# Optimization experiments

Measured on AMD Instinct MI355X. Metric: run time of the kernel, lower is better.

The kernel has to match this reference:

```python
import jax, jax.numpy as jnp
import numpy as np
from jax import lax

B, T, D = 4096, 2048, 8
NUM_LAYERS = 6  # hidden_size = 1


def setup_inputs() -> dict:
    key = jax.random.key(0)
    ks = jax.random.split(key, 6)
    u = lambda k, shape: jax.random.uniform(k, shape, jnp.float32, -1.0, 1.0)  # pytorch init: U(-1/sqrt(H), 1/sqrt(H)), H=1
    return {
        "x": jax.random.normal(ks[0], (B, T, D), jnp.float32),
        "W_ih0": u(ks[1], (3, D)),            # layer 0 input weights [3*H, D], H=1
        "W_ih_rest": u(ks[2], (NUM_LAYERS - 1, 3)),  # layers 1..5 input weights [3*H, 1] squeezed
        "W_hh": u(ks[3], (NUM_LAYERS, 3)),    # hidden weights [3*H, H] squeezed (H=1)
        "b_ih": u(ks[4], (NUM_LAYERS, 3)),
        "b_hh": u(ks[5], (NUM_LAYERS, 3)),
    }


def _gru_layer(xp, w_hh, b_hh):
    # xp: [B, T, 3] precomputed input-gate projections (W_ih @ x + b_ih)
    # w_hh, b_hh: [3] scalar hidden weights/biases (hidden_size == 1)
    def step(h, xp_t):  # h: [B], xp_t: [B, 3]
        r = jax.nn.sigmoid(xp_t[:, 0] + w_hh[0] * h + b_hh[0])
        z = jax.nn.sigmoid(xp_t[:, 1] + w_hh[1] * h + b_hh[1])
        n = jnp.tanh(xp_t[:, 2] + r * (w_hh[2] * h + b_hh[2]))
        h_new = (1.0 - z) * n + z * h
        return h_new, h_new

    h0 = jnp.zeros(xp.shape[0], xp.dtype)
    _, ys = lax.scan(step, h0, jnp.swapaxes(xp, 0, 1))  # ys: [T, B]
    return jnp.swapaxes(ys, 0, 1)  # [B, T]


def reference(x, W_ih0, W_ih_rest, W_hh, b_ih, b_hh):
    # Layer 0: project D-dim input to the 3 gates once, then scan over time.
    xp = jnp.einsum('btd,gd->btg', x, W_ih0) + b_ih[0]  # [B, T, 3]
    h_seq = _gru_layer(xp, W_hh[0], b_hh[0])            # [B, T]
    # Layers 1..5: scalar input (previous layer's hidden), hidden_size=1.
    # Dropout(0.5) between layers is inference-mode identity here.
    for l in range(1, NUM_LAYERS):
        xp = h_seq[:, :, None] * W_ih_rest[l - 1][None, None, :] + b_ih[l]  # [B, T, 3]
        h_seq = _gru_layer(xp, W_hh[l], b_hh[l])
    # y[:, -1, 0] -> last timestep of last layer
    return h_seq[:, -1]
```

## Files before the change

### kernel.cpp

```cpp
#include <hip/hip_runtime.h>


#define T_LEN 2048
#define T8    (T_LEN * 8)
#define NCH   256

typedef __attribute__((ext_vector_type(2))) float v2f;

__device__ __forceinline__ float dpp_shr1(float v) {
    int i = __builtin_bit_cast(int, v);
    int r = __builtin_amdgcn_update_dpp(0, i, 0x111, 0xF, 0xF, true);
    return __builtin_bit_cast(float, r);
}

#define DPPSHL(S, v) __builtin_bit_cast(float,                                \
    __builtin_amdgcn_update_dpp(0, __builtin_bit_cast(int, (v)),              \
                                0x100 | ((S) == 0 ? 1 : (S)), 0xF, 0xF, true))
#define DPPSHLX(S, v) ((S) == 0 ? (v) : DPPSHL(S, v))

__global__ __launch_bounds__(64)
__attribute__((amdgpu_waves_per_eu(1, 1)))
void gru_scan(const float* __restrict__ x,
              const float* __restrict__ Wih0,
              const float* __restrict__ Wrest,
              const float* __restrict__ Whh,
              const float* __restrict__ bih,
              const float* __restrict__ bhh,
              float* __restrict__ out)
{
    const int lane = threadIdx.x & 63;
    const int l    = lane & 7;
    const int g    = lane >> 3;
    const int b    = blockIdx.x * 8 + g;

    const float c1 = -1.44269504088896340736f;
    const float cz =  1.44269504088896340736f;
    const float c2 = 2.0f * c1;

    const int  lidx = l < 6 ? l : 5;
    const bool lz   = (l == 0);
    const float m1  = lz ? 0.0f : 1.0f;

    const float whpr = c1 * Whh[lidx * 3 + 0];
    const float whpz = cz * Whh[lidx * 3 + 1];
    const float whpn = c2 * Whh[lidx * 3 + 2];
    const float bhpn = c2 * bhh[lidx * 3 + 2];
    const v2f  WH12 = {whpr, whpz};

    const int ir = lidx >= 1 ? lidx - 1 : 0;
    const float W1r = m1 * c1 * Wrest[ir * 3 + 0];
    const float W1z = m1 * cz * Wrest[ir * 3 + 1];
    const float W1n = m1 * c2 * Wrest[ir * 3 + 2];
    const v2f  W1rz = {W1r, W1z};
    const float B1r = c1 * (bih[lidx * 3 + 0] + bhh[lidx * 3 + 0]);
    const float B1z = cz * (bih[lidx * 3 + 1] + bhh[lidx * 3 + 1]);
    const float B1n = c2 *  bih[lidx * 3 + 2];
    const v2f  B1rz = {B1r, B1z};

    const v2f  B0rz = {c1 * (bih[0] + bhh[0]), cz * (bih[1] + bhh[1])};
    const float B0n = c2 * bih[2];
    v2f  wrz[8];
    float wn[8];
    #pragma unroll
    for (int d = 0; d < 8; ++d) {
        wrz[d] = (v2f){c1 * Wih0[d], cz * Wih0[8 + d]};
        wn[d]  = c2 * Wih0[16 + d];
    }

    const float4* xp = reinterpret_cast<const float4*>(x + (size_t)b * T8) + (lane & 7) * 2;

    float4 L0a, L0b, L1a, L1b, L2a, L2b, L3a, L3b;
    v2f   PZArz, PZBrz;
    float PZAn,  PZBn;
    v2f   SrzA[8], SrzB[8];
    float SnA[8],  SnB[8];
    float h = 0.0f;

#define LOADL(A, B, C)                                                        \
    { const int cc_ = ((C) < NCH) ? (C) : 0;                                  \
      const float4* p_ = xp + (size_t)cc_ * 16;                               \
      A = p_[0]; B = p_[1]; }

#define GETF(S, A, B) ((S)==0?(A).x:(S)==1?(A).y:(S)==2?(A).z:(S)==3?(A).w:  \
                       (S)==4?(B).x:(S)==5?(B).y:(S)==6?(B).z:(B).w)

#define DOT_SLICE(S, LA, LB, PRZ, PN)                                         \
    { const float xv_ = GETF(S, LA, LB);                                      \
      if ((S) == 0) { PRZ = wrz[0] * (v2f){xv_, xv_} + B0rz;                  \
                      PN  = fmaf(xv_, wn[0], B0n); }                          \
      else          { PRZ = wrz[S] * (v2f){xv_, xv_} + PRZ;                   \
                      PN  = fmaf(xv_, wn[S], PN); } }

#define PRESEL(S, SRZ, SN, PRZs, PNs)                                         \
    { const float br_ = DPPSHLX(S, (PRZs).x);                                 \
      const float bz_ = DPPSHLX(S, (PRZs).y);                                 \
      const float bn_ = DPPSHLX(S, (PNs));                                    \
      SRZ[S] = (v2f){lz ? br_ : B1r, lz ? bz_ : B1z};                         \
      SN[S]  = lz ? bn_ : B1n; }

    auto step1 = [&](int i, v2f brz, float bn, bool guard) {
        const float nbr = dpp_shr1(h);

        const v2f t12 = WH12 * (v2f){h, h} + brz;
        const v2f arz = W1rz * (v2f){nbr, nbr} + t12;
        const float er = __builtin_amdgcn_exp2f(arz.x);
        const float ez = __builtin_amdgcn_exp2f(arz.y);
        const float r  = __builtin_amdgcn_rcpf(1.0f + er);
        const float pz1 = 1.0f + ez;

        const v2f tnx = (v2f){whpn, W1n} * (v2f){h, nbr} + (v2f){bhpn, bn};
        const float na = fmaf(r, tnx.x, tnx.y);
        const float en = __builtin_amdgcn_exp2f(na);

        const float P  = fmaf(en, pz1, pz1);
        const float R  = __builtin_amdgcn_rcpf(P);
        const float hp1 = h + 1.0f;
        const float hm1 = 1.0f - h;
        const float q  = fmaf(-hp1, en, hm1);
        const float hn = fmaf(R, q, h);

        if (guard) {
            h = ((unsigned)(i - l) < (unsigned)T_LEN) ? hn : h;
        } else {
            h = hn;
        }
    };

#define STEPX(S, C, SRr, SNr, SRw, SNw, PZr_rz, PZr_n, PZw_rz, PZw_n,         \
              LNa, LNb, GD)                                                   \
    { step1((C) * 8 + (S), SRr[S], SNr[S], GD);                               \
      DOT_SLICE(S, LNa, LNb, PZw_rz, PZw_n)                                   \
      PRESEL(S, SRw, SNw, PZr_rz, PZr_n) }

#define RUN_CHUNK(C, SRr, SNr, SRw, SNw, PZr_rz, PZr_n, PZw_rz, PZw_n,        \
                  LNa, LNb, LlA, LlB, C4, GD)                                 \
    { LOADL(LlA, LlB, C4)                                                     \
      STEPX(0, C, SRr, SNr, SRw, SNw, PZr_rz, PZr_n, PZw_rz, PZw_n, LNa, LNb, GD) \
      STEPX(1, C, SRr, SNr, SRw, SNw, PZr_rz, PZr_n, PZw_rz, PZw_n, LNa, LNb, GD) \
      STEPX(2, C, SRr, SNr, SRw, SNw, PZr_rz, PZr_n, PZw_rz, PZw_n, LNa, LNb, GD) \
      STEPX(3, C, SRr, SNr, SRw, SNw, PZr_rz, PZr_n, PZw_rz, PZw_n, LNa, LNb, GD) \
      STEPX(4, C, SRr, SNr, SRw, SNw, PZr_rz, PZr_n, PZw_rz, PZw_n, LNa, LNb, GD) \
      STEPX(5, C, SRr, SNr, SRw, SNw, PZr_rz, PZr_n, PZw_rz, PZw_n, LNa, LNb, GD) \
      STEPX(6, C, SRr, SNr, SRw, SNw, PZr_rz, PZr_n, PZw_rz, PZw_n, LNa, LNb, GD) \
      STEPX(7, C, SRr, SNr, SRw, SNw, PZr_rz, PZr_n, PZw_rz, PZw_n, LNa, LNb, GD) }

    LOADL(L0a, L0b, 0) LOADL(L1a, L1b, 1) LOADL(L2a, L2b, 2) LOADL(L3a, L3b, 3)

    DOT_SLICE(0, L0a, L0b, PZArz, PZAn) DOT_SLICE(1, L0a, L0b, PZArz, PZAn)
    DOT_SLICE(2, L0a, L0b, PZArz, PZAn) DOT_SLICE(3, L0a, L0b, PZArz, PZAn)
    DOT_SLICE(4, L0a, L0b, PZArz, PZAn) DOT_SLICE(5, L0a, L0b, PZArz, PZAn)
    DOT_SLICE(6, L0a, L0b, PZArz, PZAn) DOT_SLICE(7, L0a, L0b, PZArz, PZAn)

    DOT_SLICE(0, L1a, L1b, PZBrz, PZBn) DOT_SLICE(1, L1a, L1b, PZBrz, PZBn)
    DOT_SLICE(2, L1a, L1b, PZBrz, PZBn) DOT_SLICE(3, L1a, L1b, PZBrz, PZBn)
    DOT_SLICE(4, L1a, L1b, PZBrz, PZBn) DOT_SLICE(5, L1a, L1b, PZBrz, PZBn)
    DOT_SLICE(6, L1a, L1b, PZBrz, PZBn) DOT_SLICE(7, L1a, L1b, PZBrz, PZBn)

    PRESEL(0, SrzA, SnA, PZArz, PZAn) PRESEL(1, SrzA, SnA, PZArz, PZAn)
    PRESEL(2, SrzA, SnA, PZArz, PZAn) PRESEL(3, SrzA, SnA, PZArz, PZAn)
    PRESEL(4, SrzA, SnA, PZArz, PZAn) PRESEL(5, SrzA, SnA, PZArz, PZAn)
    PRESEL(6, SrzA, SnA, PZArz, PZAn) PRESEL(7, SrzA, SnA, PZArz, PZAn)

    RUN_CHUNK(0, SrzA, SnA, SrzB, SnB, PZBrz, PZBn, PZArz, PZAn, L2a, L2b, L0a, L0b, 4, true)
    RUN_CHUNK(1, SrzB, SnB, SrzA, SnA, PZArz, PZAn, PZBrz, PZBn, L3a, L3b, L1a, L1b, 5, false)
    RUN_CHUNK(2, SrzA, SnA, SrzB, SnB, PZBrz, PZBn, PZArz, PZAn, L0a, L0b, L2a, L2b, 6, false)
    RUN_CHUNK(3, SrzB, SnB, SrzA, SnA, PZArz, PZAn, PZBrz, PZBn, L1a, L1b, L3a, L3b, 7, false)

    #pragma unroll 1
    for (int q = 1; q < 64; ++q) {
        const int c0 = q * 4;
        RUN_CHUNK(c0 + 0, SrzA, SnA, SrzB, SnB, PZBrz, PZBn, PZArz, PZAn, L2a, L2b, L0a, L0b, c0 + 4, false)
        RUN_CHUNK(c0 + 1, SrzB, SnB, SrzA, SnA, PZArz, PZAn, PZBrz, PZBn, L3a, L3b, L1a, L1b, c0 + 5, false)
        RUN_CHUNK(c0 + 2, SrzA, SnA, SrzB, SnB, PZBrz, PZBn, PZArz, PZAn, L0a, L0b, L2a, L2b, c0 + 6, false)
        RUN_CHUNK(c0 + 3, SrzB, SnB, SrzA, SnA, PZArz, PZAn, PZBrz, PZBn, L1a, L1b, L3a, L3b, c0 + 7, false)
    }

    #pragma unroll
    for (int i = T_LEN; i < T_LEN + 5; ++i) step1(i, B1rz, B1n, true);

    if (l == 5) out[b] = h;
}

extern "C" void kernel_launch(void* const* d_in, const int* in_sizes, int n_in,
                              void* d_out, int out_size, void* d_ws, size_t ws_size,
                              hipStream_t stream) {
    const float* x     = (const float*)d_in[0];
    const float* Wih0  = (const float*)d_in[1];
    const float* Wrest = (const float*)d_in[2];
    const float* Whh   = (const float*)d_in[3];
    const float* bih   = (const float*)d_in[4];
    const float* bhh   = (const float*)d_in[5];
    float* out = (float*)d_out;

    gru_scan<<<512, 64, 0, stream>>>(x, Wih0, Wrest, Whh, bih, bhh, out);
}
```

Baseline: 148.4 us.

## Interleave two independent batch sequences per wave to hide recurrence latency

Each wave now runs two batch groups (b and b+2048) at once, interleaving their GRU step chains so the dependent exp/rcp latency of one chain can overlap the other. The grid is halved to 256 blocks. This targets the serial-dependency latency bound of the scan. In exchange it doubles register pressure, and having fewer waves may leave CUs idle on a 256-CU part. Some dead macro definitions are defined and then immediately undefined.

```diff
diff --git a/kernel.cpp b/kernel.cpp
--- a/kernel.cpp
+++ b/kernel.cpp
@@ -31,7 +31,8 @@
     const int lane = threadIdx.x & 63;
     const int l    = lane & 7;
     const int g    = lane >> 3;
-    const int b    = blockIdx.x * 8 + g;
+    const int bA   = blockIdx.x * 8 + g;
+    const int bB   = bA + 2048;
 
     const float c1 = -1.44269504088896340736f;
     const float cz =  1.44269504088896340736f;
@@ -67,18 +68,20 @@
         wn[d]  = c2 * Wih0[16 + d];
     }
 
-    const float4* xp = reinterpret_cast<const float4*>(x + (size_t)b * T8) + (lane & 7) * 2;
-
-    float4 L0a, L0b, L1a, L1b, L2a, L2b, L3a, L3b;
-    v2f   PZArz, PZBrz;
-    float PZAn,  PZBn;
-    v2f   SrzA[8], SrzB[8];
-    float SnA[8],  SnB[8];
-    float h = 0.0f;
-
-#define LOADL(A, B, C)                                                        \
+    const float4* xpA = reinterpret_cast<const float4*>(x + (size_t)bA * T8) + (lane & 7) * 2;
+    const float4* xpB = reinterpret_cast<const float4*>(x + (size_t)bB * T8) + (lane & 7) * 2;
+
+    float4 LA0a, LA0b, LA1a, LA1b, LA2a, LA2b, LA3a, LA3b;
+    float4 LB0a, LB0b, LB1a, LB1b, LB2a, LB2b, LB3a, LB3b;
+    v2f   PZAArz, PZABrz, PZBArz, PZBBrz;
+    float PZAAn,  PZABn,  PZBAn,  PZBBn;
+    v2f   SrzAA[8], SrzAB[8], SrzBA[8], SrzBB[8];
+    float SnAA[8],  SnAB[8],  SnBA[8],  SnBB[8];
+    float hA = 0.0f, hB = 0.0f;
+
+#define LOADL(P, A, B, C)                                                     \
     { const int cc_ = ((C) < NCH) ? (C) : 0;                                  \
-      const float4* p_ = xp + (size_t)cc_ * 16;                               \
+      const float4* p_ = P + (size_t)cc_ * 16;                                \
       A = p_[0]; B = p_[1]; }
 
 #define GETF(S, A, B) ((S)==0?(A).x:(S)==1?(A).y:(S)==2?(A).z:(S)==3?(A).w:  \
@@ -98,87 +101,162 @@
       SRZ[S] = (v2f){lz ? br_ : B1r, lz ? bz_ : B1z};                         \
       SN[S]  = lz ? bn_ : B1n; }
 
-    auto step1 = [&](int i, v2f brz, float bn, bool guard) {
-        const float nbr = dpp_shr1(h);
-
-        const v2f t12 = WH12 * (v2f){h, h} + brz;
-        const v2f arz = W1rz * (v2f){nbr, nbr} + t12;
-        const float er = __builtin_amdgcn_exp2f(arz.x);
-        const float ez = __builtin_amdgcn_exp2f(arz.y);
-        const float r  = __builtin_amdgcn_rcpf(1.0f + er);
-        const float pz1 = 1.0f + ez;
-
-        const v2f tnx = (v2f){whpn, W1n} * (v2f){h, nbr} + (v2f){bhpn, bn};
-        const float na = fmaf(r, tnx.x, tnx.y);
-        const float en = __builtin_amdgcn_exp2f(na);
-
-        const float P  = fmaf(en, pz1, pz1);
-        const float R  = __builtin_amdgcn_rcpf(P);
-        const float hp1 = h + 1.0f;
-        const float hm1 = 1.0f - h;
-        const float q  = fmaf(-hp1, en, hm1);
-        const float hn = fmaf(R, q, h);
+    auto step2 = [&](int i, v2f brzA, float bnA, v2f brzB, float bnB, bool guard) {
+        const float nbrA = dpp_shr1(hA);
+        const float nbrB = dpp_shr1(hB);
+
+        const v2f t12A = WH12 * (v2f){hA, hA} + brzA;
+        const v2f t12B = WH12 * (v2f){hB, hB} + brzB;
+        const v2f arzA = W1rz * (v2f){nbrA, nbrA} + t12A;
+        const v2f arzB = W1rz * (v2f){nbrB, nbrB} + t12B;
+
+        const float erA = __builtin_amdgcn_exp2f(arzA.x);
+        const float erB = __builtin_amdgcn_exp2f(arzB.x);
+        const float ezA = __builtin_amdgcn_exp2f(arzA.y);
+        const float ezB = __builtin_amdgcn_exp2f(arzB.y);
+        const float rA  = __builtin_amdgcn_rcpf(1.0f + erA);
+        const float rB  = __builtin_amdgcn_rcpf(1.0f + erB);
+        const float pz1A = 1.0f + ezA;
+        const float pz1B = 1.0f + ezB;
+
+        const v2f tnxA = (v2f){whpn, W1n} * (v2f){hA, nbrA} + (v2f){bhpn, bnA};
+        const v2f tnxB = (v2f){whpn, W1n} * (v2f){hB, nbrB} + (v2f){bhpn, bnB};
+        const float naA = fmaf(rA, tnxA.x, tnxA.y);
+        const float naB = fmaf(rB, tnxB.x, tnxB.y);
+        const float enA = __builtin_amdgcn_exp2f(naA);
+        const float enB = __builtin_amdgcn_exp2f(naB);
+
+        const float PA = fmaf(enA, pz1A, pz1A);
+        const float PB = fmaf(enB, pz1B, pz1B);
+        const float RA = __builtin_amdgcn_rcpf(PA);
+        const float RB = __builtin_amdgcn_rcpf(PB);
+
+        const float hp1A = hA + 1.0f;
+        const float hp1B = hB + 1.0f;
+        const float hm1A = 1.0f - hA;
+        const float hm1B = 1.0f - hB;
+        const float qA = fmaf(-hp1A, enA, hm1A);
+        const float qB = fmaf(-hp1B, enB, hm1B);
+        const float hnA = fmaf(RA, qA, hA);
+        const float hnB = fmaf(RB, qB, hB);
 
         if (guard) {
-            h = ((unsigned)(i - l) < (unsigned)T_LEN) ? hn : h;
+            const bool ok = (unsigned)(i - l) < (unsigned)T_LEN;
+            hA = ok ? hnA : hA;
+            hB = ok ? hnB : hB;
         } else {
-            h = hn;
+            hA = hnA;
+            hB = hnB;
         }
     };
 
-#define STEPX(S, C, SRr, SNr, SRw, SNw, PZr_rz, PZr_n, PZw_rz, PZw_n,         \
-              LNa, LNb, GD)                                                   \
-    { step1((C) * 8 + (S), SRr[S], SNr[S], GD);                               \
-      DOT_SLICE(S, LNa, LNb, PZw_rz, PZw_n)                                   \
-      PRESEL(S, SRw, SNw, PZr_rz, PZr_n) }
-
-#define RUN_CHUNK(C, SRr, SNr, SRw, SNw, PZr_rz, PZr_n, PZw_rz, PZw_n,        \
-                  LNa, LNb, LlA, LlB, C4, GD)                                 \
-    { LOADL(LlA, LlB, C4)                                                     \
-      STEPX(0, C, SRr, SNr, SRw, SNw, PZr_rz, PZr_n, PZw_rz, PZw_n, LNa, LNb, GD) \
-      STEPX(1, C, SRr, SNr, SRw, SNw, PZr_rz, PZr_n, PZw_rz, PZw_n, LNa, LNb, GD) \
-      STEPX(2, C, SRr, SNr, SRw, SNw, PZr_rz, PZr_n, PZw_rz, PZw_n, LNa, LNb, GD) \
-      STEPX(3, C, SRr, SNr, SRw, SNw, PZr_rz, PZr_n, PZw_rz, PZw_n, LNa, LNb, GD) \
-      STEPX(4, C, SRr, SNr, SRw, SNw, PZr_rz, PZr_n, PZw_rz, PZw_n, LNa, LNb, GD) \
-      STEPX(5, C, SRr, SNr, SRw, SNw, PZr_rz, PZr_n, PZw_rz, PZw_n, LNa, LNb, GD) \
-      STEPX(6, C, SRr, SNr, SRw, SNw, PZr_rz, PZr_n, PZw_rz, PZw_n, LNa, LNb, GD) \
-      STEPX(7, C, SRr, SNr, SRw, SNw, PZr_rz, PZr_n, PZw_rz, PZw_n, LNa, LNb, GD) }
-
-    LOADL(L0a, L0b, 0) LOADL(L1a, L1b, 1) LOADL(L2a, L2b, 2) LOADL(L3a, L3b, 3)
-
-    DOT_SLICE(0, L0a, L0b, PZArz, PZAn) DOT_SLICE(1, L0a, L0b, PZArz, PZAn)
-    DOT_SLICE(2, L0a, L0b, PZArz, PZAn) DOT_SLICE(3, L0a, L0b, PZArz, PZAn)
-    DOT_SLICE(4, L0a, L0b, PZArz, PZAn) DOT_SLICE(5, L0a, L0b, PZArz, PZAn)
-    DOT_SLICE(6, L0a, L0b, PZArz, PZAn) DOT_SLICE(7, L0a, L0b, PZArz, PZAn)
-
-    DOT_SLICE(0, L1a, L1b, PZBrz, PZBn) DOT_SLICE(1, L1a, L1b, PZBrz, PZBn)
-    DOT_SLICE(2, L1a, L1b, PZBrz, PZBn) DOT_SLICE(3, L1a, L1b, PZBrz, PZBn)
-    DOT_SLICE(4, L1a, L1b, PZBrz, PZBn) DOT_SLICE(5, L1a, L1b, PZBrz, PZBn)
-    DOT_SLICE(6, L1a, L1b, PZBrz, PZBn) DOT_SLICE(7, L1a, L1b, PZBrz, PZBn)
-
-    PRESEL(0, SrzA, SnA, PZArz, PZAn) PRESEL(1, SrzA, SnA, PZArz, PZAn)
-    PRESEL(2, SrzA, SnA, PZArz, PZAn) PRESEL(3, SrzA, SnA, PZArz, PZAn)
-    PRESEL(4, SrzA, SnA, PZArz, PZAn) PRESEL(5, SrzA, SnA, PZArz, PZAn)
-    PRESEL(6, SrzA, SnA, PZArz, PZAn) PRESEL(7, SrzA, SnA, PZArz, PZAn)
-
-    RUN_CHUNK(0, SrzA, SnA, SrzB, SnB, PZBrz, PZBn, PZArz, PZAn, L2a, L2b, L0a, L0b, 4, true)
-    RUN_CHUNK(1, SrzB, SnB, SrzA, SnA, PZArz, PZAn, PZBrz, PZBn, L3a, L3b, L1a, L1b, 5, false)
-    RUN_CHUNK(2, SrzA, SnA, SrzB, SnB, PZBrz, PZBn, PZArz, PZAn, L0a, L0b, L2a, L2b, 6, false)
-    RUN_CHUNK(3, SrzB, SnB, SrzA, SnA, PZArz, PZAn, PZBrz, PZBn, L1a, L1b, L3a, L3b, 7, false)
+#define STEPX2(S, C, Sb, So, GD)                                              \
+    { step2((C) * 8 + (S), SrzA##Sb[S], SnA##Sb[S], SrzB##Sb[S], SnB##Sb[S], GD); \
+      DOT_SLICE(S, LA##Sb##a_, LA##Sb##b_, PZA##Sb##rz_, PZA##Sb##n_)         \
+      PRESEL(S, SrzA##So, SnA##So, PZA##So##rz_, PZA##So##n_)                 \
+      DOT_SLICE(S, LB##Sb##a_, LB##Sb##b_, PZB##Sb##rz_, PZB##Sb##n_)         \
+      PRESEL(S, SrzB##So, SnB##So, PZB##So##rz_, PZB##So##n_) }
+
+#define RUN_CHUNK2(C, RD, WR, LN, LL, C4, GD)                                 \
+    { LOADL(xpA, LA##LL##a, LA##LL##b, C4)                                    \
+      LOADL(xpB, LB##LL##a, LB##LL##b, C4)                                    \
+      STEPX2_ALL(C, RD, WR, LN, GD) }
+
+#define STEPX2_ALL(C, RD, WR, LN, GD)                                         \
+    { auto& LA##RD##a_ = LA##LN##a; auto& LA##RD##b_ = LA##LN##b;             \
+      auto& LB##RD##a_ = LB##LN##a; auto& LB##RD##b_ = LB##LN##b;             \
+      auto& PZA##RD##rz_ = PZA##RD##rz; auto& PZA##RD##n_ = PZA##RD##n;       \
+      auto& PZB##RD##rz_ = PZB##RD##rz; auto& PZB##RD##n_ = PZB##RD##n;       \
+      auto& PZA##WR##rz_ = PZA##WR##rz; auto& PZA##WR##n_ = PZA##WR##n;       \
+      auto& PZB##WR##rz_ = PZB##WR##rz; auto& PZB##WR##n_ = PZB##WR##n;       \
+      STEPX2_8(C, RD, WR, GD) }
+
+#undef STEPX2
+#undef RUN_CHUNK2
+#undef STEPX2_ALL
+
+#define FSTEP(S, C, SRZA, SNA, SRZB, SNB,                    \
+              LNAa, LNAb, LNBa, LNBb, PZWArz, PZWAn, PZWBrz, PZWBn, \
+              SWA, SWNA, SWB, SWNB, PZRArz, PZRAn, PZRBrz, PZRBn,  \
+              GD)                                                             \
+    { step2((C) * 8 + (S), SRZA[S], SNA[S], SRZB[S], SNB[S], GD);             \
+      DOT_SLICE(S, LNAa, LNAb, PZWArz, PZWAn)                                 \
+      DOT_SLICE(S, LNBa, LNBb, PZWBrz, PZWBn)                                 \
+      PRESEL(S, SWA, SWNA, PZRArz, PZRAn)                                     \
+      PRESEL(S, SWB, SWNB, PZRBrz, PZRBn) }
+
+#define RUNC(C, SRZA, SNA, SRZB, SNB, LNAa, LNAb, LNBa, LNBb,                 \
+             PZWArz, PZWAn, PZWBrz, PZWBn, SWA, SWNA, SWB, SWNB,              \
+             PZRArz, PZRAn, PZRBrz, PZRBn, LLAa, LLAb, LLBa, LLBb, C4, GD)    \
+    { LOADL(xpA, LLAa, LLAb, C4) LOADL(xpB, LLBa, LLBb, C4)                   \
+      FSTEP(0, C, SRZA, SNA, SRZB, SNB, LNAa, LNAb, LNBa, LNBb, PZWArz, PZWAn, PZWBrz, PZWBn, SWA, SWNA, SWB, SWNB, PZRArz, PZRAn, PZRBrz, PZRBn, GD) \
+      FSTEP(1, C, SRZA, SNA, SRZB, SNB, LNAa, LNAb, LNBa, LNBb, PZWArz, PZWAn, PZWBrz, PZWBn, SWA, SWNA, SWB, SWNB, PZRArz, PZRAn, PZRBrz, PZRBn, GD) \
+      FSTEP(2, C, SRZA, SNA, SRZB, SNB, LNAa, LNAb, LNBa, LNBb, PZWArz, PZWAn, PZWBrz, PZWBn, SWA, SWNA, SWB, SWNB, PZRArz, PZRAn, PZRBrz, PZRBn, GD) \
+      FSTEP(3, C, SRZA, SNA, SRZB, SNB, LNAa, LNAb, LNBa, LNBb, PZWArz, PZWAn, PZWBrz, PZWBn, SWA, SWNA, SWB, SWNB, PZRArz, PZRAn, PZRBrz, PZRBn, GD) \
+      FSTEP(4, C, SRZA, SNA, SRZB, SNB, LNAa, LNAb, LNBa, LNBb, PZWArz, PZWAn, PZWBrz, PZWBn, SWA, SWNA, SWB, SWNB, PZRArz, PZRAn, PZRBrz, PZRBn, GD) \
+      FSTEP(5, C, SRZA, SNA, SRZB, SNB, LNAa, LNAb, LNBa, LNBb, PZWArz, PZWAn, PZWBrz, PZWBn, SWA, SWNA, SWB, SWNB, PZRArz, PZRAn, PZRBrz, PZRBn, GD) \
+      FSTEP(6, C, SRZA, SNA, SRZB, SNB, LNAa, LNAb, LNBa, LNBb, PZWArz, PZWAn, PZWBrz, PZWBn, SWA, SWNA, SWB, SWNB, PZRArz, PZRAn, PZRBrz, PZRBn, GD) \
+      FSTEP(7, C, SRZA, SNA, SRZB, SNB, LNAa, LNAb, LNBa, LNBb, PZWArz, PZWAn, PZWBrz, PZWBn, SWA, SWNA, SWB, SWNB, PZRArz, PZRAn, PZRBrz, PZRBn, GD) }
+
+    LOADL(xpA, LA0a, LA0b, 0) LOADL(xpB, LB0a, LB0b, 0)
+    LOADL(xpA, LA1a, LA1b, 1) LOADL(xpB, LB1a, LB1b, 1)
+    LOADL(xpA, LA2a, LA2b, 2) LOADL(xpB, LB2a, LB2b, 2)
+    LOADL(xpA, LA3a, LA3b, 3) LOADL(xpB, LB3a, LB3b, 3)
+
+#define DOT8(LA, LB, PRZ, PN)                                                 \
+    DOT_SLICE(0, LA, LB, PRZ, PN) DOT_SLICE(1, LA, LB, PRZ, PN)               \
+    DOT_SLICE(2, LA, LB, PRZ, PN) DOT_SLICE(3, LA, LB, PRZ, PN)               \
+    DOT_SLICE(4, LA, LB, PRZ, PN) DOT_SLICE(5, LA, LB, PRZ, PN)               \
+    DOT_SLICE(6, LA, LB, PRZ, PN) DOT_SLICE(7, LA, LB, PRZ, PN)
+
+#define PRESEL8(SRZ, SN, PRZ, PN)                                             \
+    PRESEL(0, SRZ, SN, PRZ, PN) PRESEL(1, SRZ, SN, PRZ, PN)                   \
+    PRESEL(2, SRZ, SN, PRZ, PN) PRESEL(3, SRZ, SN, PRZ, PN)                   \
+    PRESEL(4, SRZ, SN, PRZ, PN) PRESEL(5, SRZ, SN, PRZ, PN)                   \
+    PRESEL(6, SRZ, SN, PRZ, PN) PRESEL(7, SRZ, SN, PRZ, PN)
+
+    DOT8(LA0a, LA0b, PZAArz, PZAAn) DOT8(LB0a, LB0b, PZBArz, PZBAn)
+    DOT8(LA1a, LA1b, PZABrz, PZABn) DOT8(LB1a, LB1b, PZBBrz, PZBBn)
+    PRESEL8(SrzAA, SnAA, PZAArz, PZAAn) PRESEL8(SrzBA, SnBA, PZBArz, PZBAn)
+
+    RUNC(0, SrzAA, SnAA, SrzBA, SnBA, LA2a, LA2b, LB2a, LB2b,
+         PZAArz, PZAAn, PZBArz, PZBAn, SrzAB, SnAB, SrzBB, SnBB,
+         PZABrz, PZABn, PZBBrz, PZBBn, LA0a, LA0b, LB0a, LB0b, 4, true)
+    RUNC(1, SrzAB, SnAB, SrzBB, SnBB, LA3a, LA3b, LB3a, LB3b,
+         PZABrz, PZABn, PZBBrz, PZBBn, SrzAA, SnAA, SrzBA, SnBA,
+         PZAArz, PZAAn, PZBArz, PZBAn, LA1a, LA1b, LB1a, LB1b, 5, false)
+    RUNC(2, SrzAA, SnAA, SrzBA, SnBA, LA0a, LA0b, LB0a, LB0b,
+         PZAArz, PZAAn, PZBArz, PZBAn, SrzAB, SnAB, SrzBB, SnBB,
+         PZABrz, PZABn, PZBBrz, PZBBn, LA2a, LA2b, LB2a, LB2b, 6, false)
+    RUNC(3, SrzAB, SnAB, SrzBB, SnBB, LA1a, LA1b, LB1a, LB1b,
+         PZABrz, PZABn, PZBBrz, PZBBn, SrzAA, SnAA, SrzBA, SnBA,
+         PZAArz, PZAAn, PZBArz, PZBAn, LA3a, LA3b, LB3a, LB3b, 7, false)
 
     #pragma unroll 1
     for (int q = 1; q < 64; ++q) {
         const int c0 = q * 4;
-        RUN_CHUNK(c0 + 0, SrzA, SnA, SrzB, SnB, PZBrz, PZBn, PZArz, PZAn, L2a, L2b, L0a, L0b, c0 + 4, false)
-        RUN_CHUNK(c0 + 1, SrzB, SnB, SrzA, SnA, PZArz, PZAn, PZBrz, PZBn, L3a, L3b, L1a, L1b, c0 + 5, false)
-        RUN_CHUNK(c0 + 2, SrzA, SnA, SrzB, SnB, PZBrz, PZBn, PZArz, PZAn, L0a, L0b, L2a, L2b, c0 + 6, false)
-        RUN_CHUNK(c0 + 3, SrzB, SnB, SrzA, SnA, PZArz, PZAn, PZBrz, PZBn, L1a, L1b, L3a, L3b, c0 + 7, false)
+        RUNC(c0 + 0, SrzAA, SnAA, SrzBA, SnBA, LA2a, LA2b, LB2a, LB2b,
+             PZAArz, PZAAn, PZBArz, PZBAn, SrzAB, SnAB, SrzBB, SnBB,
+             PZABrz, PZABn, PZBBrz, PZBBn, LA0a, LA0b, LB0a, LB0b, c0 + 4, false)
+        RUNC(c0 + 1, SrzAB, SnAB, SrzBB, SnBB, LA3a, LA3b, LB3a, LB3b,
+             PZABrz, PZABn, PZBBrz, PZBBn, SrzAA, SnAA, SrzBA, SnBA,
+             PZAArz, PZAAn, PZBArz, PZBAn, LA1a, LA1b, LB1a, LB1b, c0 + 5, false)
+        RUNC(c0 + 2, SrzAA, SnAA, SrzBA, SnBA, LA0a, LA0b, LB0a, LB0b,
+             PZAArz, PZAAn, PZBArz, PZBAn, SrzAB, SnAB, SrzBB, SnBB,
+             PZABrz, PZABn, PZBBrz, PZBBn, LA2a, LA2b, LB2a, LB2b, c0 + 6, false)
+        RUNC(c0 + 3, SrzAB, SnAB, SrzBB, SnBB, LA1a, LA1b, LB1a, LB1b,
+             PZABrz, PZABn, PZBBrz, PZBBn, SrzAA, SnAA, SrzBA, SnBA,
+             PZAArz, PZAAn, PZBArz, PZBAn, LA3a, LA3b, LB3a, LB3b, c0 + 7, false)
     }
 
     #pragma unroll
-    for (int i = T_LEN; i < T_LEN + 5; ++i) step1(i, B1rz, B1n, true);
-
-    if (l == 5) out[b] = h;
+    for (int i = T_LEN; i < T_LEN + 5; ++i)
+        step2(i, B1rz, B1n, B1rz, B1n, true);
+
+    if (l == 5) {
+        out[bA] = hA;
+        out[bB] = hB;
+    }
 }
 
 extern "C" void kernel_launch(void* const* d_in, const int* in_sizes, int n_in,
@@ -192,5 +270,5 @@
     const float* bhh   = (const float*)d_in[5];
     float* out = (float*)d_out;
 
-    gru_scan<<<512, 64, 0, stream>>>(x, Wih0, Wrest, Whh, bih, bhh, out);
+    gru_scan<<<256, 64, 0, stream>>>(x, Wih0, Wrest, Whh, bih, bhh, out);
 }
```

Result: slower. 270.3 us (+82.2%).
